# Performance work log

Hardware: AMD Instinct MI355X
Metric: run time of the kernel (lower is better)

Reference implementation:

```python
import jax, jax.numpy as jnp
import numpy as np

HID = 256
VOCAB = 1000
REPEAT = 32
ALPHA = 1.0
LBR = 0.2
THRESH = 0.8 * ALPHA * (1.0 - LBR)  # 0.64


def _lstm_layer(x, Wih, Whh, bih, bhh):
    # x: [B,S,D]; returns hidden states [S,B,H] (torch gate order i,f,g,o)
    B = x.shape[0]
    H = Whh.shape[1]
    xg = jnp.einsum('bsd,gd->sbg', x, Wih) + (bih + bhh)  # [S,B,4H]
    def step(carry, gx):
        h, c = carry
        g = gx + h @ Whh.T
        i, f, gg, o = jnp.split(g, 4, axis=-1)
        c = jax.nn.sigmoid(f) * c + jax.nn.sigmoid(i) * jnp.tanh(gg)
        h = jax.nn.sigmoid(o) * jnp.tanh(c)
        return (h, c), h
    init = (jnp.zeros((B, H), x.dtype), jnp.zeros((B, H), x.dtype))
    _, hs = jax.lax.scan(step, init, xg)
    return hs


def _encode(x, Wih0, Whh0, bih0, bhh0, Wih1, Whh1, bih1, bhh1):
    # 2-layer LSTM (dropout inactive at inference), then sum over time -> [B,H]
    hs = _lstm_layer(x, Wih0, Whh0, bih0, bhh0)                      # [S,B,H]
    hs = _lstm_layer(jnp.transpose(hs, (1, 0, 2)), Wih1, Whh1, bih1, bhh1)
    return hs.sum(0)


def setup_inputs():
    key = jax.random.key(0)
    ks = jax.random.split(key, 20)
    B, S, D, H, P = 64, 128, 64, HID, 1024
    s = jnp.float32(0.05)
    return {
        'x1': jax.random.normal(ks[0], (B, S, D), jnp.float32),
        'x2': jax.random.normal(ks[1], (B, S, D), jnp.float32),
        'Wih0': s * jax.random.normal(ks[2], (4 * H, D), jnp.float32),
        'Whh0': s * jax.random.normal(ks[3], (4 * H, H), jnp.float32),
        'bih0': s * jax.random.normal(ks[4], (4 * H,), jnp.float32),
        'bhh0': s * jax.random.normal(ks[5], (4 * H,), jnp.float32),
        'Wih1': s * jax.random.normal(ks[6], (4 * H, H), jnp.float32),
        'Whh1': s * jax.random.normal(ks[7], (4 * H, H), jnp.float32),
        'bih1': s * jax.random.normal(ks[8], (4 * H,), jnp.float32),
        'bhh1': s * jax.random.normal(ks[9], (4 * H,), jnp.float32),
        'fc1_w': s * jax.random.normal(ks[10], (P, 2 * H), jnp.float32),
        'fc1_b': s * jax.random.normal(ks[11], (P,), jnp.float32),
        'fc2_w': s * jax.random.normal(ks[12], (P, P), jnp.float32),
        'fc2_b': s * jax.random.normal(ks[13], (P,), jnp.float32),
        'fc3_w': s * jax.random.normal(ks[14], (VOCAB * REPEAT, P), jnp.float32),
        'fc3_b': s * jax.random.normal(ks[15], (VOCAB * REPEAT,), jnp.float32),
        'bn_g': jnp.ones((P,), jnp.float32),
        'bn_b': jnp.zeros((P,), jnp.float32),
    }


def reference(x1, x2, Wih0, Whh0, bih0, bhh0, Wih1, Whh1, bih1, bhh1,
              fc1_w, fc1_b, fc2_w, fc2_b, fc3_w, fc3_b, bn_g, bn_b):
    out1 = _encode(x1, Wih0, Whh0, bih0, bhh0, Wih1, Whh1, bih1, bhh1)
    out2 = _encode(x2, Wih0, Whh0, bih0, bhh0, Wih1, Whh1, bih1, bhh1)
    h = jnp.concatenate([out1, out2], axis=1)                # [B,2H]
    h = jax.nn.gelu(h @ fc1_w.T + fc1_b, approximate=False)  # exact gelu (torch)
    h = h + jax.nn.relu(h @ fc2_w.T + fc2_b)
    # BatchNorm1d with batch statistics (training-mode normalization)
    mu = h.mean(0)
    var = h.var(0)
    h = (h - mu) / jnp.sqrt(var + 1e-5) * bn_g + bn_b
    scores = jax.nn.relu(h @ fc3_w.T + fc3_b)
    scores = scores.reshape(-1, VOCAB, REPEAT)               # [B,V,R]
    # vectorized replacement of the per-row .item() selection loop:
    # number of atoms selected per row at threshold 0.8*alpha*(1-lbr)
    num_select = jnp.maximum(1, (scores > THRESH).sum(axis=(1, 2)))
    return scores, num_select
```

## Files before the change

kernel.cpp:

```cpp
#include <hip/hip_runtime.h>
#include <cmath>


typedef _Float16 f16;
typedef _Float16 f16x8 __attribute__((ext_vector_type(8)));
typedef _Float16 f16x4 __attribute__((ext_vector_type(4)));
typedef float f32x4 __attribute__((ext_vector_type(4)));

#define MFMA(a,b,c) __builtin_amdgcn_mfma_f32_16x16x32_f16((a),(b),(c),0,0,0)
#define LSTR 280

__device__ __forceinline__ float frcp(float x) { return __builtin_amdgcn_rcpf(x); }
__device__ __forceinline__ float sigf(float x)  { return frcp(1.f + __expf(-x)); }
__device__ __forceinline__ float tanhf_(float x){ return 1.f - 2.f*frcp(__expf(2.f*x) + 1.f); }

__device__ __forceinline__ void wait_flag(int* f, int target) {
    while (__hip_atomic_load(f, __ATOMIC_RELAXED, __HIP_MEMORY_SCOPE_AGENT) < target)
        __builtin_amdgcn_s_sleep(1);
    (void)__hip_atomic_load(f, __ATOMIC_ACQUIRE, __HIP_MEMORY_SCOPE_AGENT);
}

__global__ void k_convert(const float* __restrict__ x1, const float* __restrict__ x2,
                          const float* __restrict__ Wih0, const float* __restrict__ Whh0,
                          const float* __restrict__ bih0, const float* __restrict__ bhh0,
                          const float* __restrict__ Wih1, const float* __restrict__ Whh1,
                          const float* __restrict__ bih1, const float* __restrict__ bhh1,
                          f16* __restrict__ x16, f16* __restrict__ w16, float* __restrict__ bsum,
                          int* __restrict__ flg)
{
    int i = blockIdx.x * 256 + threadIdx.x;
    if (i < 524288) { x16[i] = (f16)x1[i]; x16[524288 + i] = (f16)x2[i]; }
    if (i < 65536)  w16[i] = (f16)Wih0[i];
    if (i < 262144) {
        w16[65536  + i] = (f16)Whh0[i];
        w16[327680 + i] = (f16)Wih1[i];
        w16[589824 + i] = (f16)Whh1[i];
    }
    if (i < 1024) { bsum[i] = bih0[i] + bhh0[i]; bsum[1024 + i] = bih1[i] + bhh1[i]; }
    if (i < 64) flg[i] = 0;
}

template<int K>
__global__ __launch_bounds__(512)
void k_proj(const f16* __restrict__ A, const f16* __restrict__ Bw,
            const float* __restrict__ bias, f16* __restrict__ out)
{
    const int w = threadIdx.x >> 6, lane = threadIdx.x & 63;
    const int quad = lane >> 4, l16 = lane & 15;
    const long m0 = (long)blockIdx.x * 128 + w * 16;
    f32x4 acc[2][4] = {};
    #pragma unroll
    for (int kc = 0; kc < K/32; ++kc) {
        const int ko = kc*32 + quad*8;
        f16x8 a = *(const f16x8*)(A + (m0 + l16)*K + ko);
        #pragma unroll
        for (int tg = 0; tg < 2; ++tg) {
            const int ti = blockIdx.y*2 + tg;
            #pragma unroll
            for (int g = 0; g < 4; ++g) {
                f16x8 b = *(const f16x8*)(Bw + (long)(g*256 + ti*16 + l16)*K + ko);
                acc[tg][g] = MFMA(a, b, acc[tg][g]);
            }
        }
    }
    #pragma unroll
    for (int tg = 0; tg < 2; ++tg) {
        const int ti = blockIdx.y*2 + tg;
        float bi[4];
        #pragma unroll
        for (int g = 0; g < 4; ++g) bi[g] = bias[g*256 + ti*16 + l16];
        #pragma unroll
        for (int r = 0; r < 4; ++r) {
            long mm = m0 + quad*4 + r;
            f16x4 pv;
            #pragma unroll
            for (int g = 0; g < 4; ++g) pv[g] = (f16)(acc[tg][g][r] + bi[g]);
            *(f16x4*)(out + mm*1024 + ti*64 + l16*4) = pv;
        }
    }
}

__global__ __launch_bounds__(512, 2)
void k_mega(const f16* __restrict__ w16, const f16* __restrict__ xg0,
            f16* __restrict__ xg1, f16* __restrict__ h0s,
            const float* __restrict__ bsum1, float* __restrict__ out_enc,
            int* __restrict__ flags)
{
    __shared__ f16 wl[256*LSTR];
    __shared__ f16 hb[2*16*LSTR];
    const int tid = threadIdx.x;
    const int w = tid >> 6, lane = tid & 63;
    const int quad = lane >> 4, l16 = lane & 15;
    const int role = blockIdx.x >> 3, g = blockIdx.x & 7;

    const f16* W = (role == 0) ? w16 + 65536
                 : (role == 1) ? w16 + 327680
                               : w16 + 589824;

    f16x8 bres[6][8];
    #pragma unroll
    for (int s6 = 0; s6 < 6; ++s6) {
        const int tile = (s6 >> 1)*16 + 2*w + (s6 & 1);
        #pragma unroll
        for (int kc = 0; kc < 8; ++kc)
            bres[s6][kc] = *(const f16x8*)(W + (tile*16 + l16)*256 + kc*32 + quad*8);
    }
    {
        const int r = tid >> 1, hh = tid & 1;
        const f16* src = W + (768 + r)*256 + hh*128;
        f16* dst = wl + r*LSTR + hh*128;
        #pragma unroll
        for (int j = 0; j < 16; ++j)
            *(f16x8*)(dst + j*8) = *(const f16x8*)(src + j*8);
    }

    if (role == 1) {
        float bi[2][4];
        #pragma unroll
        for (int q = 0; q < 2; ++q)
            #pragma unroll
            for (int g4 = 0; g4 < 4; ++g4) bi[q][g4] = bsum1[g4*256 + (2*w+q)*16 + l16];
        __syncthreads();
        #pragma unroll 1
        for (int s = 0; s < 128; ++s) {
            if ((s & 1) == 0) {
                if (tid == 0) wait_flag(&flags[g], s + 2);
                __syncthreads();
            }
            const f16* hrow = h0s + ((long)s*128 + g*16 + l16)*256 + quad*8;
            f16x8 av[8];
            #pragma unroll
            for (int kc = 0; kc < 8; ++kc) av[kc] = *(const f16x8*)(hrow + kc*32);
            #pragma unroll
            for (int q = 0; q < 2; ++q) {
                const int ti = 2*w + q;
                f32x4 ai = {}, af = {}, ag = {}, ao = {};
                #pragma unroll
                for (int kc = 0; kc < 8; ++kc) {
                    f16x8 bo = *(const f16x8*)(wl + (ti*16 + l16)*LSTR + kc*32 + quad*8);
                    ai = MFMA(av[kc], bres[q][kc],   ai);
                    af = MFMA(av[kc], bres[2+q][kc], af);
                    ag = MFMA(av[kc], bres[4+q][kc], ag);
                    ao = MFMA(av[kc], bo,            ao);
                }
                #pragma unroll
                for (int r = 0; r < 4; ++r) {
                    f16x4 pv;
                    pv[0] = (f16)(ai[r] + bi[q][0]);
                    pv[1] = (f16)(af[r] + bi[q][1]);
                    pv[2] = (f16)(ag[r] + bi[q][2]);
                    pv[3] = (f16)(ao[r] + bi[q][3]);
                    *(f16x4*)(xg1 + ((long)(g*16 + quad*4 + r)*128 + s)*1024
                                  + ti*64 + l16*4) = pv;
                }
            }
            if (s & 1) {
                __syncthreads();
                if (tid == 0)
                    __hip_atomic_store(&flags[8+g], s + 1, __ATOMIC_RELEASE,
                                       __HIP_MEMORY_SCOPE_AGENT);
            }
        }
        return;
    }

    for (int i = tid; i < 2*16*LSTR; i += 512) hb[i] = (f16)0.f;

    const f16* xg = (role == 0) ? xg0 : xg1;
    const f16* xp[4];
    #pragma unroll
    for (int r = 0; r < 4; ++r)
        xp[r] = xg + (long)(g*16 + quad*4 + r)*131072 + (2*w)*64 + l16*4;

    float c[8]    = {0,0,0,0,0,0,0,0};
    float oacc[8] = {0,0,0,0,0,0,0,0};
    __syncthreads();

    #pragma unroll 1
    for (int s = 0; s < 128; ++s) {
        const int rb = s & 1, wb = rb ^ 1;
        if (role == 2 && (s & 1) == 0) {
            if (tid == 0) wait_flag(&flags[8+g], s + 2);
            __syncthreads();
        }
        if (role == 0 && s > 0) {
            const int cc = tid >> 5, kk = (tid & 31) * 8;
            f16x8 hv = *(const f16x8*)(hb + (rb*16 + cc)*LSTR + kk);
            *(f16x8*)(h0s + ((long)(s-1)*128 + g*16 + cc)*256 + kk) = hv;
        }
        f16x4 xv[2][4];
        #pragma unroll
        for (int r = 0; r < 4; ++r) {
            xv[0][r] = *(const f16x4*)(xp[r]);
            xv[1][r] = *(const f16x4*)(xp[r] + 64);
        }
        #pragma unroll
        for (int q = 0; q < 2; ++q) {
            const int ti = 2*w + q;
            f32x4 ai = {}, af = {}, ag = {}, ao = {};
            #pragma unroll
            for (int kc = 0; kc < 8; ++kc) {
                f16x8 a  = *(const f16x8*)(hb + (rb*16 + l16)*LSTR + kc*32 + quad*8);
                f16x8 bo = *(const f16x8*)(wl + (ti*16 + l16)*LSTR + kc*32 + quad*8);
                ai = MFMA(a, bres[q][kc],   ai);
                af = MFMA(a, bres[2+q][kc], af);
                ag = MFMA(a, bres[4+q][kc], ag);
                ao = MFMA(a, bo,            ao);
            }
            #pragma unroll
            for (int r = 0; r < 4; ++r) {
                float gi = sigf(ai[r] + (float)xv[q][r][0]);
                float gf = sigf(af[r] + (float)xv[q][r][1]);
                float gg = tanhf_(ag[r] + (float)xv[q][r][2]);
                float go = sigf(ao[r] + (float)xv[q][r][3]);
                const int ci = q*4 + r;
                float cn = gf*c[ci] + gi*gg;
                c[ci] = cn;
                float hn = go * tanhf_(cn);
                if (role == 2) oacc[ci] += hn;
                hb[(wb*16 + quad*4 + r)*LSTR + ti*16 + l16] = (f16)hn;
            }
        }
        #pragma unroll
        for (int r = 0; r < 4; ++r) xp[r] += 1024;
        __syncthreads();
        if (role == 0 && (s & 1) == 0 && s > 0 && tid == 0)
            __hip_atomic_store(&flags[g], s, __ATOMIC_RELEASE,
                               __HIP_MEMORY_SCOPE_AGENT);
    }
    if (role == 0) {
        const int cc = tid >> 5, kk = (tid & 31) * 8;
        f16x8 hv = *(const f16x8*)(hb + (0*16 + cc)*LSTR + kk);
        *(f16x8*)(h0s + ((long)127*128 + g*16 + cc)*256 + kk) = hv;
        __syncthreads();
        if (tid == 0)
            __hip_atomic_store(&flags[g], 128, __ATOMIC_RELEASE,
                               __HIP_MEMORY_SCOPE_AGENT);
    }
    if (role == 2) {
        #pragma unroll
        for (int q = 0; q < 2; ++q)
            #pragma unroll
            for (int r = 0; r < 4; ++r)
                out_enc[(long)(g*16 + quad*4 + r)*256 + (2*w+q)*16 + l16] = oacc[q*4 + r];
    }
}

template<int K, int MODE>
__global__ __launch_bounds__(256)
void k_fc(const float* __restrict__ A, const float* __restrict__ W,
          const float* __restrict__ bias, const float* __restrict__ res,
          const float* __restrict__ bng, const float* __restrict__ bnb,
          float* __restrict__ out, const int Nst)
{
    __shared__ float ws[32*64];
    __shared__ float as[64*64];
    __shared__ float mus[32], rss[32];
    const int tid = threadIdx.x;
    const int n0 = blockIdx.x * 32;
    const int m2 = tid & 31, ndg = tid >> 5;
    float acc[2][4] = {};
    for (int kc = 0; kc < K/64; ++kc) {
        __syncthreads();
        {
            const int col = tid >> 3, k8 = (tid & 7)*8;
            const float* src = W + (long)(n0 + col)*K + kc*64 + k8;
            *(float4*)(ws + col*64 + k8)     = *(const float4*)(src);
            *(float4*)(ws + col*64 + k8 + 4) = *(const float4*)(src + 4);
        }
        {
            const int m = tid >> 2, j4 = (tid & 3)*16;
            #pragma unroll
            for (int i4 = 0; i4 < 4; ++i4) {
                const int kk = kc*64 + j4 + i4*4;
                const float* srcA;
                if (MODE == 0) srcA = (kk < 256) ? (A + (long)m*256 + kk)
                                                 : (A + 16384 + (long)m*256 + kk - 256);
                else           srcA = A + (long)m*K + kk;
                float4 v = *(const float4*)srcA;
                as[(j4 + i4*4 + 0)*64 + m] = v.x;
                as[(j4 + i4*4 + 1)*64 + m] = v.y;
                as[(j4 + i4*4 + 2)*64 + m] = v.z;
                as[(j4 + i4*4 + 3)*64 + m] = v.w;
            }
        }
        __syncthreads();
        #pragma unroll 4
        for (int k4 = 0; k4 < 64; k4 += 4) {
            float a0[4], a1[4];
            #pragma unroll
            for (int i = 0; i < 4; ++i) {
                a0[i] = as[(k4+i)*64 + m2];
                a1[i] = as[(k4+i)*64 + m2 + 32];
            }
            #pragma unroll
            for (int j = 0; j < 4; ++j) {
                const float4 wv = *(const float4*)(ws + (ndg*4 + j)*64 + k4);
                acc[0][j] += a0[0]*wv.x + a0[1]*wv.y + a0[2]*wv.z + a0[3]*wv.w;
                acc[1][j] += a1[0]*wv.x + a1[1]*wv.y + a1[2]*wv.z + a1[3]*wv.w;
            }
        }
    }
    if (MODE == 1) {
        float vv[2][4];
        #pragma unroll
        for (int i = 0; i < 2; ++i)
            #pragma unroll
            for (int j = 0; j < 4; ++j) {
                const int m = m2 + i*32, nn = n0 + ndg*4 + j;
                vv[i][j] = res[(long)m*1024 + nn] + fmaxf(acc[i][j] + bias[nn], 0.f);
            }
        __syncthreads();
        #pragma unroll
        for (int i = 0; i < 2; ++i)
            #pragma unroll
            for (int j = 0; j < 4; ++j)
                as[(m2 + i*32)*33 + ndg*4 + j] = vv[i][j];
        __syncthreads();
        if (tid < 32) {
            float s = 0.f, ss = 0.f;
            #pragma unroll 4
            for (int m = 0; m < 64; ++m) {
                float x = as[m*33 + tid];
                s += x; ss += x*x;
            }
            const float mu = s * (1.f/64.f);
            mus[tid] = mu;
            rss[tid] = rsqrtf(ss * (1.f/64.f) - mu*mu + 1e-5f);
        }
        __syncthreads();
        #pragma unroll
        for (int i = 0; i < 2; ++i)
            #pragma unroll
            for (int j = 0; j < 4; ++j) {
                const int m = m2 + i*32, cl = ndg*4 + j, nn = n0 + cl;
                out[(long)m*Nst + nn] = (vv[i][j] - mus[cl]) * rss[cl] * bng[nn] + bnb[nn];
            }
        return;
    }
    #pragma unroll
    for (int i = 0; i < 2; ++i) {
        const int m = m2 + i*32;
        #pragma unroll
        for (int j = 0; j < 4; ++j) {
            const int nn = n0 + ndg*4 + j;
            float v = acc[i][j] + bias[nn];
            if (MODE == 0) v = 0.5f * v * (1.0f + erff(v * 0.7071067811865475f));
            else           v = fmaxf(v, 0.f);
            out[(long)m*Nst + nn] = v;
        }
    }
}

__global__ void k_count(const float* __restrict__ scores, float* __restrict__ outc)
{
    const int row = blockIdx.x, tid = threadIdx.x;
    const float* p = scores + (long)row*32000;
    int cnt = 0;
    for (int i = tid; i < 32000; i += 256)
        cnt += ((double)p[i] > 0.6400000000000001) ? 1 : 0;
    __shared__ int red[256];
    red[tid] = cnt; __syncthreads();
    for (int off = 128; off > 0; off >>= 1) {
        if (tid < off) red[tid] += red[tid + off];
        __syncthreads();
    }
    if (tid == 0) outc[row] = (float)(red[0] < 1 ? 1 : red[0]);
}

extern "C" void kernel_launch(void* const* d_in, const int* in_sizes, int n_in,
                              void* d_out, int out_size, void* d_ws, size_t ws_size,
                              hipStream_t stream)
{
    const float* x1    = (const float*)d_in[0];
    const float* x2    = (const float*)d_in[1];
    const float* Wih0  = (const float*)d_in[2];
    const float* Whh0  = (const float*)d_in[3];
    const float* bih0  = (const float*)d_in[4];
    const float* bhh0  = (const float*)d_in[5];
    const float* Wih1  = (const float*)d_in[6];
    const float* Whh1  = (const float*)d_in[7];
    const float* bih1  = (const float*)d_in[8];
    const float* bhh1  = (const float*)d_in[9];
    const float* fc1_w = (const float*)d_in[10];
    const float* fc1_b = (const float*)d_in[11];
    const float* fc2_w = (const float*)d_in[12];
    const float* fc2_b = (const float*)d_in[13];
    const float* fc3_w = (const float*)d_in[14];
    const float* fc3_b = (const float*)d_in[15];
    const float* bn_g  = (const float*)d_in[16];
    const float* bn_b  = (const float*)d_in[17];
    float* out = (float*)d_out;

    char* ws = (char*)d_ws;
    f16*   x16   = (f16*)(ws);
    f16*   w16   = (f16*)(ws + 2097152);
    float* bsum  = (float*)(ws + 3801088);
    int*   flags = (int*)(ws + 3809280);
    float* enc   = (float*)(ws + 3809536);
    f16*   h0s   = (f16*)(ws + 3940608);
    f16*   xg0   = (f16*)(ws + 12329216);
    f16*   xg1   = (f16*)(ws + 45883648);
    float* h1    = (float*)(ws + 12329216);
    float* h3    = (float*)(ws + 12591360);

    k_convert<<<2048, 256, 0, stream>>>(x1,x2,Wih0,Whh0,bih0,bhh0,Wih1,Whh1,bih1,bhh1,
                                        x16, w16, bsum, flags);
    k_proj<64><<<dim3(128,8), 512, 0, stream>>>(x16, w16, bsum, xg0);
    k_mega<<<24, 512, 0, stream>>>(w16, xg0, xg1, h0s, bsum + 1024, enc, flags);
    k_fc<512,0><<<32, 256, 0, stream>>>(enc, fc1_w, fc1_b, nullptr, nullptr, nullptr, h1, 1024);
    k_fc<1024,1><<<32, 256, 0, stream>>>(h1, fc2_w, fc2_b, h1, bn_g, bn_b, h3, 1024);
    k_fc<1024,2><<<1000, 256, 0, stream>>>(h3, fc3_w, fc3_b, nullptr, nullptr, nullptr, out, 32000);
    k_count<<<64, 256, 0, stream>>>(out, out + 2048000);
}
```

Measured before the change: 987.4 us.

## Fuse input conversion into projection and coarsen inter-layer sync to 4 steps

The x1/x2 fp32-to-fp16 conversion moves out of k_convert and into the layer-0 projection kernel, which now reads fp32 input directly. This removes an extra pass over the inputs and shrinks the workspace. Inside the persistent LSTM kernel, the producer/consumer flag handshake between layers runs every 4 timesteps instead of every 2, and the next step's h0 rows and xg gate inputs are prefetched into registers. Hidden-state operands are also loaded once per step instead of once per tile. In exchange, register pressure rises and the downstream layers lag further behind layer 0.

```diff
diff --git a/kernel.cpp b/kernel.cpp
--- a/kernel.cpp
+++ b/kernel.cpp
@@ -20,16 +20,14 @@
     (void)__hip_atomic_load(f, __ATOMIC_ACQUIRE, __HIP_MEMORY_SCOPE_AGENT);
 }
 
-__global__ void k_convert(const float* __restrict__ x1, const float* __restrict__ x2,
-                          const float* __restrict__ Wih0, const float* __restrict__ Whh0,
+__global__ void k_convert(const float* __restrict__ Wih0, const float* __restrict__ Whh0,
                           const float* __restrict__ bih0, const float* __restrict__ bhh0,
                           const float* __restrict__ Wih1, const float* __restrict__ Whh1,
                           const float* __restrict__ bih1, const float* __restrict__ bhh1,
-                          f16* __restrict__ x16, f16* __restrict__ w16, float* __restrict__ bsum,
+                          f16* __restrict__ w16, float* __restrict__ bsum,
                           int* __restrict__ flg)
 {
     int i = blockIdx.x * 256 + threadIdx.x;
-    if (i < 524288) { x16[i] = (f16)x1[i]; x16[524288 + i] = (f16)x2[i]; }
     if (i < 65536)  w16[i] = (f16)Wih0[i];
     if (i < 262144) {
         w16[65536  + i] = (f16)Whh0[i];
@@ -40,10 +38,11 @@
     if (i < 64) flg[i] = 0;
 }
 
-template<int K>
+template<int K, bool CVT>
 __global__ __launch_bounds__(512)
-void k_proj(const f16* __restrict__ A, const f16* __restrict__ Bw,
-            const float* __restrict__ bias, f16* __restrict__ out)
+void k_proj(const void* __restrict__ A0v, const void* __restrict__ A1v,
+            const f16* __restrict__ Bw, const float* __restrict__ bias,
+            f16* __restrict__ out)
 {
     const int w = threadIdx.x >> 6, lane = threadIdx.x & 63;
     const int quad = lane >> 4, l16 = lane & 15;
@@ -52,7 +51,16 @@
     #pragma unroll
     for (int kc = 0; kc < K/32; ++kc) {
         const int ko = kc*32 + quad*8;
-        f16x8 a = *(const f16x8*)(A + (m0 + l16)*K + ko);
+        f16x8 a;
+        if (CVT) {
+            const float* Af = (const float*)((m0 < 8192) ? A0v : A1v);
+            const float* ap = Af + ((m0 & 8191) + l16)*K + ko;
+            float4 v0 = *(const float4*)ap, v1 = *(const float4*)(ap + 4);
+            a[0]=(f16)v0.x; a[1]=(f16)v0.y; a[2]=(f16)v0.z; a[3]=(f16)v0.w;
+            a[4]=(f16)v1.x; a[5]=(f16)v1.y; a[6]=(f16)v1.z; a[7]=(f16)v1.w;
+        } else {
+            a = *(const f16x8*)((const f16*)A0v + (m0 + l16)*K + ko);
+        }
         #pragma unroll
         for (int tg = 0; tg < 2; ++tg) {
             const int ti = blockIdx.y*2 + tg;
@@ -121,16 +129,24 @@
             #pragma unroll
             for (int g4 = 0; g4 < 4; ++g4) bi[q][g4] = bsum1[g4*256 + (2*w+q)*16 + l16];
         __syncthreads();
+        f16x8 av[8], avn[8];
         #pragma unroll 1
         for (int s = 0; s < 128; ++s) {
-            if ((s & 1) == 0) {
-                if (tid == 0) wait_flag(&flags[g], s + 2);
+            if ((s & 3) == 0) {
+                if (tid == 0) wait_flag(&flags[g], s + 4);
                 __syncthreads();
-            }
-            const f16* hrow = h0s + ((long)s*128 + g*16 + l16)*256 + quad*8;
-            f16x8 av[8];
-            #pragma unroll
-            for (int kc = 0; kc < 8; ++kc) av[kc] = *(const f16x8*)(hrow + kc*32);
+                const f16* hrow = h0s + ((long)s*128 + g*16 + l16)*256 + quad*8;
+                #pragma unroll
+                for (int kc = 0; kc < 8; ++kc) av[kc] = *(const f16x8*)(hrow + kc*32);
+            } else {
+                #pragma unroll
+                for (int kc = 0; kc < 8; ++kc) av[kc] = avn[kc];
+            }
+            if (((s+1) & 3) != 0) {
+                const f16* hrow = h0s + ((long)(s+1)*128 + g*16 + l16)*256 + quad*8;
+                #pragma unroll
+                for (int kc = 0; kc < 8; ++kc) avn[kc] = *(const f16x8*)(hrow + kc*32);
+            }
             #pragma unroll
             for (int q = 0; q < 2; ++q) {
                 const int ti = 2*w + q;
@@ -154,7 +170,7 @@
                                   + ti*64 + l16*4) = pv;
                 }
             }
-            if (s & 1) {
+            if ((s & 3) == 3) {
                 __syncthreads();
                 if (tid == 0)
                     __hip_atomic_store(&flags[8+g], s + 1, __ATOMIC_RELEASE,
@@ -174,38 +190,55 @@
 
     float c[8]    = {0,0,0,0,0,0,0,0};
     float oacc[8] = {0,0,0,0,0,0,0,0};
+    f16x4 xv[2][4], xvn[2][4];
     __syncthreads();
 
     #pragma unroll 1
     for (int s = 0; s < 128; ++s) {
         const int rb = s & 1, wb = rb ^ 1;
-        if (role == 2 && (s & 1) == 0) {
-            if (tid == 0) wait_flag(&flags[8+g], s + 2);
+        if (role == 2 && (s & 3) == 0) {
+            if (tid == 0) wait_flag(&flags[8+g], s + 4);
             __syncthreads();
+        }
+        const bool fresh = (role == 2) ? ((s & 3) == 0) : (s == 0);
+        if (fresh) {
+            #pragma unroll
+            for (int r = 0; r < 4; ++r) {
+                xv[0][r] = *(const f16x4*)(xp[r]);
+                xv[1][r] = *(const f16x4*)(xp[r] + 64);
+            }
+        } else {
+            #pragma unroll
+            for (int r = 0; r < 4; ++r) { xv[0][r] = xvn[0][r]; xv[1][r] = xvn[1][r]; }
+        }
+        const bool pf = (role == 2) ? (((s+1) & 3) != 0) : (s + 1 < 128);
+        if (pf) {
+            #pragma unroll
+            for (int r = 0; r < 4; ++r) {
+                xvn[0][r] = *(const f16x4*)(xp[r] + 1024);
+                xvn[1][r] = *(const f16x4*)(xp[r] + 1024 + 64);
+            }
         }
         if (role == 0 && s > 0) {
             const int cc = tid >> 5, kk = (tid & 31) * 8;
             f16x8 hv = *(const f16x8*)(hb + (rb*16 + cc)*LSTR + kk);
             *(f16x8*)(h0s + ((long)(s-1)*128 + g*16 + cc)*256 + kk) = hv;
         }
-        f16x4 xv[2][4];
-        #pragma unroll
-        for (int r = 0; r < 4; ++r) {
-            xv[0][r] = *(const f16x4*)(xp[r]);
-            xv[1][r] = *(const f16x4*)(xp[r] + 64);
-        }
+        f16x8 av[8];
+        #pragma unroll
+        for (int kc = 0; kc < 8; ++kc)
+            av[kc] = *(const f16x8*)(hb + (rb*16 + l16)*LSTR + kc*32 + quad*8);
         #pragma unroll
         for (int q = 0; q < 2; ++q) {
             const int ti = 2*w + q;
             f32x4 ai = {}, af = {}, ag = {}, ao = {};
             #pragma unroll
             for (int kc = 0; kc < 8; ++kc) {
-                f16x8 a  = *(const f16x8*)(hb + (rb*16 + l16)*LSTR + kc*32 + quad*8);
                 f16x8 bo = *(const f16x8*)(wl + (ti*16 + l16)*LSTR + kc*32 + quad*8);
-                ai = MFMA(a, bres[q][kc],   ai);
-                af = MFMA(a, bres[2+q][kc], af);
-                ag = MFMA(a, bres[4+q][kc], ag);
-                ao = MFMA(a, bo,            ao);
+                ai = MFMA(av[kc], bres[q][kc],   ai);
+                af = MFMA(av[kc], bres[2+q][kc], af);
+                ag = MFMA(av[kc], bres[4+q][kc], ag);
+                ao = MFMA(av[kc], bo,            ao);
             }
             #pragma unroll
             for (int r = 0; r < 4; ++r) {
@@ -224,7 +257,7 @@
         #pragma unroll
         for (int r = 0; r < 4; ++r) xp[r] += 1024;
         __syncthreads();
-        if (role == 0 && (s & 1) == 0 && s > 0 && tid == 0)
+        if (role == 0 && (s & 3) == 0 && s > 0 && tid == 0)
             __hip_atomic_store(&flags[g], s, __ATOMIC_RELEASE,
                                __HIP_MEMORY_SCOPE_AGENT);
     }
@@ -393,20 +426,19 @@
     float* out = (float*)d_out;
 
     char* ws = (char*)d_ws;
-    f16*   x16   = (f16*)(ws);
-    f16*   w16   = (f16*)(ws + 2097152);
-    float* bsum  = (float*)(ws + 3801088);
-    int*   flags = (int*)(ws + 3809280);
-    float* enc   = (float*)(ws + 3809536);
-    f16*   h0s   = (f16*)(ws + 3940608);
-    f16*   xg0   = (f16*)(ws + 12329216);
-    f16*   xg1   = (f16*)(ws + 45883648);
-    float* h1    = (float*)(ws + 12329216);
-    float* h3    = (float*)(ws + 12591360);
-
-    k_convert<<<2048, 256, 0, stream>>>(x1,x2,Wih0,Whh0,bih0,bhh0,Wih1,Whh1,bih1,bhh1,
-                                        x16, w16, bsum, flags);
-    k_proj<64><<<dim3(128,8), 512, 0, stream>>>(x16, w16, bsum, xg0);
+    f16*   w16   = (f16*)(ws);
+    float* bsum  = (float*)(ws + 1703936);
+    int*   flags = (int*)(ws + 1712128);
+    float* enc   = (float*)(ws + 1712384);
+    f16*   h0s   = (f16*)(ws + 1843456);
+    f16*   xg0   = (f16*)(ws + 10232064);
+    f16*   xg1   = (f16*)(ws + 43786496);
+    float* h1    = (float*)(ws + 10232064);
+    float* h3    = (float*)(ws + 10494208);
+
+    k_convert<<<1024, 256, 0, stream>>>(Wih0,Whh0,bih0,bhh0,Wih1,Whh1,bih1,bhh1,
+                                        w16, bsum, flags);
+    k_proj<64,true><<<dim3(128,8), 512, 0, stream>>>(x1, x2, w16, bsum, xg0);
     k_mega<<<24, 512, 0, stream>>>(w16, xg0, xg1, h0s, bsum + 1024, enc, flags);
     k_fc<512,0><<<32, 256, 0, stream>>>(enc, fc1_w, fc1_b, nullptr, nullptr, nullptr, h1, 1024);
     k_fc<1024,1><<<32, 256, 0, stream>>>(h1, fc2_w, fc2_b, h1, bn_g, bn_b, h3, 1024);
```

After: 1.215 ms. +23.1%, slower.
